# Kernel optimization log

Measured on AMD Instinct MI355X. Metric: run time of the kernel, lower is better.

## Reference

```python
import jax, jax.numpy as jnp
import numpy as np

N_NODES = 50000
N_EDGES = 1000000
IN_DIM = 256
N_ETYPE = 1000
L1_DIM = 16


def setup_inputs() -> dict:
    key = jax.random.key(0)
    ks = jax.random.split(key, 7)
    z = jax.random.normal(ks[0], (N_NODES, IN_DIM), dtype=jnp.float32)
    edge_index = jax.random.randint(ks[1], (2, N_EDGES), 0, N_NODES, dtype=jnp.int64)
    edge_type = jax.random.randint(ks[2], (N_EDGES,), 0, N_ETYPE, dtype=jnp.int64)
    w1_l1 = jax.random.normal(ks[3], (IN_DIM, L1_DIM), dtype=jnp.float32)
    w2_l1 = jax.random.normal(ks[4], (IN_DIM, L1_DIM), dtype=jnp.float32)
    std = 1.0 / np.sqrt(L1_DIM)
    w1_l2 = jax.random.normal(ks[5], (N_ETYPE, L1_DIM), dtype=jnp.float32) * std
    w2_l2 = jax.random.normal(ks[6], (N_ETYPE, L1_DIM), dtype=jnp.float32) * std
    return {"z": z, "edge_index": edge_index, "edge_type": edge_type,
            "w1_l1": w1_l1, "w1_l2": w1_l2, "w2_l1": w2_l1, "w2_l2": w2_l2}


def reference(z, edge_index, edge_type, w1_l1, w1_l2, w2_l1, w2_l2):
    # gather source/target node feats: [E, in_dim]
    d1 = jax.nn.relu(z[edge_index[0]] @ w1_l1)  # [E, l1_dim]
    d2 = jax.nn.relu(z[edge_index[1]] @ w2_l1)  # [E, l1_dim]
    s1 = jnp.sum(d1 * w1_l2[edge_type], axis=1)  # [E]
    s2 = jnp.sum(d2 * w2_l2[edge_type], axis=1)  # [E]
    return jax.nn.sigmoid(s1 + s2)
```

## Files before the change

kernel.cpp:

```cpp
#include <hip/hip_runtime.h>
#include <hip/hip_fp16.h>
#include <math.h>

#define IN_DIM 256
#define L1_DIM 16
#define N_ETYPE_MAX 1000

typedef _Float16 f16x8 __attribute__((ext_vector_type(8)));
typedef float f32x4 __attribute__((ext_vector_type(4)));

__global__ __launch_bounds__(256) void proj_kernel(
    const float* __restrict__ z,
    const float* __restrict__ w1,
    const float* __restrict__ w2,
    const float* __restrict__ w1_l2,
    const float* __restrict__ w2_l2,
    __half* __restrict__ h1,
    __half* __restrict__ h2,
    __half* __restrict__ wq,
    int n_nodes, int n_l2, int nblocks_proj) {
  if ((int)blockIdx.x >= nblocks_proj) {
    int t0 = ((int)blockIdx.x - nblocks_proj) * 256 + (int)threadIdx.x;
    for (int i = t0; i < n_l2; i += 8 * 256) {
      int t = i >> 4;
      int j = i & 15;
      wq[t * 32 + j]      = __float2half(w1_l2[i]);
      wq[t * 32 + 16 + j] = __float2half(w2_l2[i]);
    }
    return;
  }

  const int tid  = (int)threadIdx.x;
  const int lane = tid & 63;
  const int wv   = tid >> 6;
  const int r    = lane & 15;
  const int q    = lane >> 4;
  const int node0 = (int)blockIdx.x * 64;

  f16x8 bf1[8], bf2[8];
#pragma unroll
  for (int s = 0; s < 8; ++s) {
#pragma unroll
    for (int j = 0; j < 8; ++j) {
      int k = 32 * s + 8 * q + j;
      bf1[s][j] = (_Float16)w1[k * L1_DIM + r];
      bf2[s][j] = (_Float16)w2[k * L1_DIM + r];
    }
  }

  int arow = node0 + wv * 16 + r;
  int ar = arow < n_nodes ? arow : (n_nodes - 1);
  const float* zrow = z + (size_t)ar * IN_DIM + 8 * q;

  f32x4 acc1 = {0.f, 0.f, 0.f, 0.f};
  f32x4 acc2 = {0.f, 0.f, 0.f, 0.f};

#pragma unroll
  for (int s = 0; s < 8; ++s) {
    float4 lo = *reinterpret_cast<const float4*>(zrow + 32 * s);
    float4 hi = *reinterpret_cast<const float4*>(zrow + 32 * s + 4);
    f16x8 af;
    af[0] = (_Float16)lo.x; af[1] = (_Float16)lo.y;
    af[2] = (_Float16)lo.z; af[3] = (_Float16)lo.w;
    af[4] = (_Float16)hi.x; af[5] = (_Float16)hi.y;
    af[6] = (_Float16)hi.z; af[7] = (_Float16)hi.w;
    acc1 = __builtin_amdgcn_mfma_f32_16x16x32_f16(af, bf1[s], acc1, 0, 0, 0);
    acc2 = __builtin_amdgcn_mfma_f32_16x16x32_f16(af, bf2[s], acc2, 0, 0, 0);
  }

#pragma unroll
  for (int i = 0; i < 4; ++i) {
    int node = node0 + wv * 16 + 4 * q + i;
    if (node < n_nodes) {
      h1[(size_t)node * L1_DIM + r] = __float2half(fmaxf(acc1[i], 0.f));
      h2[(size_t)node * L1_DIM + r] = __float2half(fmaxf(acc2[i], 0.f));
    }
  }
}

union F4H { float4 f; __half2 h[4]; };

__global__ __launch_bounds__(512) void edge_kernel(
    const int* __restrict__ edge_index,
    const int* __restrict__ edge_type,
    const __half* __restrict__ h1,
    const __half* __restrict__ h2,
    const __half* __restrict__ wq,
    float* __restrict__ out,
    int n_edges, int n_types) {
  __shared__ __align__(16) __half wl[N_ETYPE_MAX * 32];

  const int tid = (int)threadIdx.x;

  {
    const float4* src = reinterpret_cast<const float4*>(wq);
    float4* dst = reinterpret_cast<float4*>(wl);
    int nf4 = n_types * 4;
    for (int i = tid; i < nf4; i += 512) dst[i] = src[i];
  }
  __syncthreads();

  const int q = tid & 1;
  const int pair = tid >> 1;
  const int stride = (int)gridDim.x * 256;

  for (int e = (int)blockIdx.x * 256 + pair; e < n_edges; e += stride) {
    int src = edge_index[e];
    int dst = edge_index[n_edges + e];
    int t   = edge_type[e];

    F4H a, b, u, v;
    a.f = *reinterpret_cast<const float4*>(h1 + (size_t)src * L1_DIM + q * 8);
    b.f = *reinterpret_cast<const float4*>(h2 + (size_t)dst * L1_DIM + q * 8);
    u.f = *reinterpret_cast<const float4*>(wl + t * 32 + q * 8);
    v.f = *reinterpret_cast<const float4*>(wl + t * 32 + 16 + q * 8);

    float s = 0.f;
#if __has_builtin(__builtin_amdgcn_fdot2)
#pragma unroll
    for (int p = 0; p < 4; ++p) {
      s = __builtin_amdgcn_fdot2(a.h[p], u.h[p], s, false);
      s = __builtin_amdgcn_fdot2(b.h[p], v.h[p], s, false);
    }
#else
#pragma unroll
    for (int p = 0; p < 4; ++p) {
      float2 af = __half22float2(a.h[p]), uf = __half22float2(u.h[p]);
      float2 bf = __half22float2(b.h[p]), vf = __half22float2(v.h[p]);
      s = fmaf(af.x, uf.x, s); s = fmaf(af.y, uf.y, s);
      s = fmaf(bf.x, vf.x, s); s = fmaf(bf.y, vf.y, s);
    }
#endif

    s += __shfl_xor(s, 1);
    if (q == 0) {
      out[e] = 1.0f / (1.0f + __expf(-s));
    }
  }
}

extern "C" void kernel_launch(void* const* d_in, const int* in_sizes, int n_in,
                              void* d_out, int out_size, void* d_ws, size_t ws_size,
                              hipStream_t stream) {
  const float* z      = (const float*)d_in[0];
  const int* edge_idx = (const int*)d_in[1];
  const int* edge_typ = (const int*)d_in[2];
  const float* w1_l1  = (const float*)d_in[3];
  const float* w1_l2  = (const float*)d_in[4];
  const float* w2_l1  = (const float*)d_in[5];
  const float* w2_l2  = (const float*)d_in[6];
  float* out = (float*)d_out;

  int n_nodes = in_sizes[0] / IN_DIM;
  int n_edges = in_sizes[2];
  int n_l2    = in_sizes[4];
  int n_types = n_l2 / L1_DIM;

  __half* h1 = (__half*)d_ws;
  __half* h2 = h1 + (size_t)n_nodes * L1_DIM;
  __half* wq = h2 + (size_t)n_nodes * L1_DIM;

  {
    int nblocks_proj = (n_nodes + 63) / 64;
    int grid = nblocks_proj + 8;
    proj_kernel<<<grid, 256, 0, stream>>>(z, w1_l1, w2_l1, w1_l2, w2_l2,
                                          h1, h2, wq,
                                          n_nodes, n_l2, nblocks_proj);
  }
  {
    edge_kernel<<<512, 512, 0, stream>>>(edge_idx, edge_typ, h1, h2, wq,
                                         out, n_edges, n_types);
  }
}
```

Measured before the change: 34.51 us.

## Fuse projection and edge kernels into one persistent kernel with grid barrier

Merges the node projection and edge scoring kernels into a single persistent launch of 512 blocks. Blocks first convert the layer-2 weights straight into shared memory and compute projections over strided row blocks, then meet at an atomic-counter grid barrier before the edge phase. This removes one kernel launch boundary and the global round trip for the converted weights. In exchange it adds a memset launch and a spin barrier that requires all 512 blocks to be resident at once. The projection phase also runs with fewer waves than before.

```diff
diff --git a/kernel.cpp b/kernel.cpp
--- a/kernel.cpp
+++ b/kernel.cpp
@@ -5,37 +5,43 @@
 #define IN_DIM 256
 #define L1_DIM 16
 #define N_ETYPE_MAX 1000
+#define NBLOCKS 512
+#define NTHREADS 512
 
 typedef _Float16 f16x8 __attribute__((ext_vector_type(8)));
 typedef float f32x4 __attribute__((ext_vector_type(4)));
 
-__global__ __launch_bounds__(256) void proj_kernel(
+union F4H { float4 f; __half2 h[4]; };
+
+__global__ __launch_bounds__(NTHREADS, 4) void fused_kernel(
     const float* __restrict__ z,
     const float* __restrict__ w1,
     const float* __restrict__ w2,
     const float* __restrict__ w1_l2,
     const float* __restrict__ w2_l2,
+    const int* __restrict__ edge_index,
+    const int* __restrict__ edge_type,
     __half* __restrict__ h1,
     __half* __restrict__ h2,
-    __half* __restrict__ wq,
-    int n_nodes, int n_l2, int nblocks_proj) {
-  if ((int)blockIdx.x >= nblocks_proj) {
-    int t0 = ((int)blockIdx.x - nblocks_proj) * 256 + (int)threadIdx.x;
-    for (int i = t0; i < n_l2; i += 8 * 256) {
-      int t = i >> 4;
-      int j = i & 15;
-      wq[t * 32 + j]      = __float2half(w1_l2[i]);
-      wq[t * 32 + 16 + j] = __float2half(w2_l2[i]);
-    }
-    return;
+    unsigned int* __restrict__ cnt,
+    float* __restrict__ out,
+    int n_nodes, int n_edges, int n_l2) {
+  __shared__ __align__(16) __half wl[N_ETYPE_MAX * 32];
+
+  const int tid = (int)threadIdx.x;
+  const int bid = (int)blockIdx.x;
+
+  for (int i = tid; i < n_l2; i += NTHREADS) {
+    int t = i >> 4;
+    int j = i & 15;
+    wl[t * 32 + j]      = __float2half(w1_l2[i]);
+    wl[t * 32 + 16 + j] = __float2half(w2_l2[i]);
   }
 
-  const int tid  = (int)threadIdx.x;
   const int lane = tid & 63;
   const int wv   = tid >> 6;
   const int r    = lane & 15;
   const int q    = lane >> 4;
-  const int node0 = (int)blockIdx.x * 64;
 
   f16x8 bf1[8], bf2[8];
 #pragma unroll
@@ -48,72 +54,63 @@
     }
   }
 
-  int arow = node0 + wv * 16 + r;
-  int ar = arow < n_nodes ? arow : (n_nodes - 1);
-  const float* zrow = z + (size_t)ar * IN_DIM + 8 * q;
+  const int gw = bid * 8 + wv;
+  const int n_rb = (n_nodes + 15) >> 4;
+  for (int rb = gw; rb < n_rb; rb += NBLOCKS * 8) {
+    int arow = rb * 16 + r;
+    int ar = arow < n_nodes ? arow : (n_nodes - 1);
+    const float* zrow = z + (size_t)ar * IN_DIM + 8 * q;
 
-  f32x4 acc1 = {0.f, 0.f, 0.f, 0.f};
-  f32x4 acc2 = {0.f, 0.f, 0.f, 0.f};
+    f32x4 acc1 = {0.f, 0.f, 0.f, 0.f};
+    f32x4 acc2 = {0.f, 0.f, 0.f, 0.f};
 
 #pragma unroll
-  for (int s = 0; s < 8; ++s) {
-    float4 lo = *reinterpret_cast<const float4*>(zrow + 32 * s);
-    float4 hi = *reinterpret_cast<const float4*>(zrow + 32 * s + 4);
-    f16x8 af;
-    af[0] = (_Float16)lo.x; af[1] = (_Float16)lo.y;
-    af[2] = (_Float16)lo.z; af[3] = (_Float16)lo.w;
-    af[4] = (_Float16)hi.x; af[5] = (_Float16)hi.y;
-    af[6] = (_Float16)hi.z; af[7] = (_Float16)hi.w;
-    acc1 = __builtin_amdgcn_mfma_f32_16x16x32_f16(af, bf1[s], acc1, 0, 0, 0);
-    acc2 = __builtin_amdgcn_mfma_f32_16x16x32_f16(af, bf2[s], acc2, 0, 0, 0);
+    for (int s = 0; s < 8; ++s) {
+      float4 lo = *reinterpret_cast<const float4*>(zrow + 32 * s);
+      float4 hi = *reinterpret_cast<const float4*>(zrow + 32 * s + 4);
+      f16x8 af;
+      af[0] = (_Float16)lo.x; af[1] = (_Float16)lo.y;
+      af[2] = (_Float16)lo.z; af[3] = (_Float16)lo.w;
+      af[4] = (_Float16)hi.x; af[5] = (_Float16)hi.y;
+      af[6] = (_Float16)hi.z; af[7] = (_Float16)hi.w;
+      acc1 = __builtin_amdgcn_mfma_f32_16x16x32_f16(af, bf1[s], acc1, 0, 0, 0);
+      acc2 = __builtin_amdgcn_mfma_f32_16x16x32_f16(af, bf2[s], acc2, 0, 0, 0);
+    }
+
+#pragma unroll
+    for (int i = 0; i < 4; ++i) {
+      int node = rb * 16 + 4 * q + i;
+      if (node < n_nodes) {
+        h1[(size_t)node * L1_DIM + r] = __float2half(fmaxf(acc1[i], 0.f));
+        h2[(size_t)node * L1_DIM + r] = __float2half(fmaxf(acc2[i], 0.f));
+      }
+    }
   }
 
-#pragma unroll
-  for (int i = 0; i < 4; ++i) {
-    int node = node0 + wv * 16 + 4 * q + i;
-    if (node < n_nodes) {
-      h1[(size_t)node * L1_DIM + r] = __float2half(fmaxf(acc1[i], 0.f));
-      h2[(size_t)node * L1_DIM + r] = __float2half(fmaxf(acc2[i], 0.f));
+  __syncthreads();
+  if (tid == 0) {
+    __hip_atomic_fetch_add(cnt, 1u, __ATOMIC_RELEASE, __HIP_MEMORY_SCOPE_AGENT);
+    while (__hip_atomic_load(cnt, __ATOMIC_ACQUIRE, __HIP_MEMORY_SCOPE_AGENT)
+           < (unsigned int)NBLOCKS) {
+      __builtin_amdgcn_s_sleep(8);
     }
-  }
-}
-
-union F4H { float4 f; __half2 h[4]; };
-
-__global__ __launch_bounds__(512) void edge_kernel(
-    const int* __restrict__ edge_index,
-    const int* __restrict__ edge_type,
-    const __half* __restrict__ h1,
-    const __half* __restrict__ h2,
-    const __half* __restrict__ wq,
-    float* __restrict__ out,
-    int n_edges, int n_types) {
-  __shared__ __align__(16) __half wl[N_ETYPE_MAX * 32];
-
-  const int tid = (int)threadIdx.x;
-
-  {
-    const float4* src = reinterpret_cast<const float4*>(wq);
-    float4* dst = reinterpret_cast<float4*>(wl);
-    int nf4 = n_types * 4;
-    for (int i = tid; i < nf4; i += 512) dst[i] = src[i];
   }
   __syncthreads();
 
-  const int q = tid & 1;
+  const int eq   = tid & 1;
   const int pair = tid >> 1;
-  const int stride = (int)gridDim.x * 256;
+  const int estride = NBLOCKS * (NTHREADS / 2);
 
-  for (int e = (int)blockIdx.x * 256 + pair; e < n_edges; e += stride) {
+  for (int e = bid * (NTHREADS / 2) + pair; e < n_edges; e += estride) {
     int src = edge_index[e];
     int dst = edge_index[n_edges + e];
     int t   = edge_type[e];
 
     F4H a, b, u, v;
-    a.f = *reinterpret_cast<const float4*>(h1 + (size_t)src * L1_DIM + q * 8);
-    b.f = *reinterpret_cast<const float4*>(h2 + (size_t)dst * L1_DIM + q * 8);
-    u.f = *reinterpret_cast<const float4*>(wl + t * 32 + q * 8);
-    v.f = *reinterpret_cast<const float4*>(wl + t * 32 + 16 + q * 8);
+    a.f = *reinterpret_cast<const float4*>(h1 + (size_t)src * L1_DIM + eq * 8);
+    b.f = *reinterpret_cast<const float4*>(h2 + (size_t)dst * L1_DIM + eq * 8);
+    u.f = *reinterpret_cast<const float4*>(wl + t * 32 + eq * 8);
+    v.f = *reinterpret_cast<const float4*>(wl + t * 32 + 16 + eq * 8);
 
     float s = 0.f;
 #if __has_builtin(__builtin_amdgcn_fdot2)
@@ -133,7 +130,7 @@
 #endif
 
     s += __shfl_xor(s, 1);
-    if (q == 0) {
+    if (eq == 0) {
       out[e] = 1.0f / (1.0f + __expf(-s));
     }
   }
@@ -154,21 +151,14 @@
   int n_nodes = in_sizes[0] / IN_DIM;
   int n_edges = in_sizes[2];
   int n_l2    = in_sizes[4];
-  int n_types = n_l2 / L1_DIM;
 
   __half* h1 = (__half*)d_ws;
   __half* h2 = h1 + (size_t)n_nodes * L1_DIM;
-  __half* wq = h2 + (size_t)n_nodes * L1_DIM;
+  unsigned int* cnt = (unsigned int*)(h2 + (size_t)n_nodes * L1_DIM);
 
-  {
-    int nblocks_proj = (n_nodes + 63) / 64;
-    int grid = nblocks_proj + 8;
-    proj_kernel<<<grid, 256, 0, stream>>>(z, w1_l1, w2_l1, w1_l2, w2_l2,
-                                          h1, h2, wq,
-                                          n_nodes, n_l2, nblocks_proj);
-  }
-  {
-    edge_kernel<<<512, 512, 0, stream>>>(edge_idx, edge_typ, h1, h2, wq,
-                                         out, n_edges, n_types);
-  }
+  hipMemsetAsync(cnt, 0, sizeof(unsigned int), stream);
+
+  fused_kernel<<<NBLOCKS, NTHREADS, 0, stream>>>(
+      z, w1_l1, w2_l1, w1_l2, w2_l2, edge_idx, edge_typ,
+      h1, h2, cnt, out, n_nodes, n_edges, n_l2);
 }
```

Result: slower. 135.5 us (+292.5%).
